# Kernel optimization log

Measured on AMD Instinct MI355X. Metric: run time of the kernel, lower is better.

## Reference

```python
import jax, jax.numpy as jnp
import numpy as np

D = 512      # model_dim
H = 8        # num_heads
HD = D // H  # head_dim = 64
S = 196      # tokens per channel (14x14 grid)
CHANNELS = np.array([2, 4, 6, 4], dtype=np.int32)  # multiplex channels per sample


def setup_inputs() -> dict:
    key = jax.random.key(0)
    ks = jax.random.split(key, 8)
    C = int(CHANNELS.sum())  # 16
    n = lambda k, shp, s=1.0: jax.random.normal(k, shp, dtype=jnp.float32) * s
    return {
        "x_query": n(ks[0], (C, S, D)),
        "x_keyval": n(ks[1], (C, S, D)),
        "pos": n(ks[2], (C, S, D)),
        "channels": CHANNELS,
        "Wq": n(ks[3], (D, D), 0.02), "bq": jnp.zeros((D,), jnp.float32),
        "Wk": n(ks[4], (D, D), 0.02), "bk": jnp.zeros((D,), jnp.float32),
        "Wv": n(ks[5], (D, D), 0.02), "bv": jnp.zeros((D,), jnp.float32),
        "Wo": n(ks[6], (D, D), 0.02), "bo": jnp.zeros((D,), jnp.float32),
    }


def reference(x_query, x_keyval, pos, channels, Wq, bq, Wk, bk, Wv, bv, Wo, bo):
    C, S_, D_ = x_query.shape
    ch = np.asarray(channels)
    # segment id per packed token; segment i has length channels[i]*S (== cu_seq_len blocks)
    seg = np.repeat(np.arange(ch.shape[0]), ch * S_)                # [T] static
    block_mask = seg[:, None] == seg[None, :]                        # [T,T] static bool

    xq = x_query.reshape(-1, D_)   # [T,D]
    xk = x_keyval.reshape(-1, D_)
    p = pos.reshape(-1, D_)

    # positional embedding fused into Q/K before projection (query_pos/key_pos)
    q = ((xq + p) @ Wq + bq).reshape(-1, H, HD)
    k = ((xk + p) @ Wk + bk).reshape(-1, H, HD)
    v = (xk @ Wv + bv).reshape(-1, H, HD)

    scale = 1.0 / np.sqrt(HD)
    scores = jnp.einsum('qhd,khd->hqk', q, k) * scale               # [H,T,T]
    scores = jnp.where(block_mask[None], scores, jnp.float32(-1e30))
    attn = jax.nn.softmax(scores, axis=-1)
    out = jnp.einsum('hqk,khd->qhd', attn, v).reshape(-1, D_)       # [T,D]
    out = out @ Wo + bo
    return out.reshape(C, S_, D_)
```

## Files before the change

kernel.cpp:

```cpp
#include <hip/hip_runtime.h>
#include <hip/hip_bf16.h>


typedef short short8 __attribute__((ext_vector_type(8)));
typedef float f32x4 __attribute__((ext_vector_type(4)));
typedef unsigned short ushort4v __attribute__((ext_vector_type(4)));

__device__ __forceinline__ unsigned short f2b(float f) {
    union { float f; unsigned int i; } x; x.f = f;
    unsigned int r = x.i + 0x7fffu + ((x.i >> 16) & 1u);
    return (unsigned short)(r >> 16);
}

#define NE 1605632
#define WE 262144
#define GS 72
#define LDA 520
#define TT 3136

__launch_bounds__(256)
__global__ void prep(const float* __restrict__ W0, const float* __restrict__ W1,
                     const float* __restrict__ W2, const float* __restrict__ W3,
                     unsigned short* __restrict__ WF) {
    const int tid = threadIdx.x;
    const float* W = blockIdx.z == 0 ? W0 : blockIdx.z == 1 ? W1 : blockIdx.z == 2 ? W2 : W3;
    unsigned short* T = WF + (size_t)blockIdx.z * WE;
    const int s = blockIdx.x * 4 + (tid >> 6);
    const int f = s >> 4, t = s & 15;
    const int lane = tid & 63, quad = lane >> 4, l16 = lane & 15;
    short8 o;
    #pragma unroll
    for (int j = 0; j < 8; ++j)
        o[j] = (short)f2b(W[(size_t)(t * 32 + quad * 8 + j) * 512 + f * 16 + l16]);
    *(short8*)(T + (size_t)s * 512 + lane * 8) = o;
}

__launch_bounds__(512)
__global__ void qkv_gemm(const float* __restrict__ xq, const float* __restrict__ xk,
                         const float* __restrict__ pos,
                         const unsigned short* __restrict__ WF,
                         const float* __restrict__ bq, const float* __restrict__ bk,
                         const float* __restrict__ bv,
                         unsigned short* __restrict__ qb, unsigned short* __restrict__ kb,
                         unsigned short* __restrict__ vb) {
    __shared__ __align__(16) unsigned short As[32 * LDA];

    const int z = blockIdx.z;
    const float* X = (z == 0) ? xq : xk;
    const bool addp = (z < 2);
    const unsigned short* WFw = WF + (size_t)z * WE;
    const float* bias = (z == 0) ? bq : (z == 1) ? bk : bv;
    unsigned short* C = (z == 0) ? qb : (z == 1) ? kb : vb;

    const int m0 = blockIdx.x * 32;
    const int tid = threadIdx.x;

    #pragma unroll
    for (int p = 0; p < 4; ++p) {
        const int row = p * 8 + (tid >> 6);
        const int col = (tid & 63) * 8;
        const float* src = X + (size_t)(m0 + row) * 512 + col;
        f32x4 a = *(const f32x4*)(src);
        f32x4 b = *(const f32x4*)(src + 4);
        if (addp) {
            const float* ps = pos + (size_t)(m0 + row) * 512 + col;
            f32x4 pa = *(const f32x4*)(ps), pb = *(const f32x4*)(ps + 4);
            #pragma unroll
            for (int j = 0; j < 4; ++j) { a[j] += pa[j]; b[j] += pb[j]; }
        }
        short8 o;
        #pragma unroll
        for (int j = 0; j < 4; ++j) {
            o[j] = (short)f2b(a[j]); o[4 + j] = (short)f2b(b[j]);
        }
        *(short8*)(As + row * LDA + col) = o;
    }
    __syncthreads();

    const int wave = tid >> 6, lane = tid & 63;
    const int quad = lane >> 4, l16 = lane & 15;
    const int n0 = wave * 64;
    const unsigned short* Ar0 = As + l16 * LDA + quad * 8;
    const unsigned short* Bb = WFw + (size_t)lane * 8 + (size_t)n0 * 512;

    f32x4 acc0[4] = {}, acc1[4] = {};
    short8 a0 = *(const short8*)(Ar0);
    short8 a1 = *(const short8*)(Ar0 + 16 * LDA);
    short8 b0 = *(const short8*)(Bb);
    short8 b1 = *(const short8*)(Bb + (size_t)16 * 512);
    short8 b2 = *(const short8*)(Bb + (size_t)32 * 512);
    short8 b3 = *(const short8*)(Bb + (size_t)48 * 512);
    #pragma unroll
    for (int t = 0; t < 16; ++t) {
        short8 na0, na1, nb0, nb1, nb2, nb3;
        if (t < 15) {
            na0 = *(const short8*)(Ar0 + (t + 1) * 32);
            na1 = *(const short8*)(Ar0 + 16 * LDA + (t + 1) * 32);
            nb0 = *(const short8*)(Bb + (size_t)(t + 1) * 512);
            nb1 = *(const short8*)(Bb + (size_t)(16 + t + 1) * 512);
            nb2 = *(const short8*)(Bb + (size_t)(32 + t + 1) * 512);
            nb3 = *(const short8*)(Bb + (size_t)(48 + t + 1) * 512);
        }
        acc0[0] = __builtin_amdgcn_mfma_f32_16x16x32_bf16(a0, b0, acc0[0], 0, 0, 0);
        acc1[0] = __builtin_amdgcn_mfma_f32_16x16x32_bf16(a1, b0, acc1[0], 0, 0, 0);
        acc0[1] = __builtin_amdgcn_mfma_f32_16x16x32_bf16(a0, b1, acc0[1], 0, 0, 0);
        acc1[1] = __builtin_amdgcn_mfma_f32_16x16x32_bf16(a1, b1, acc1[1], 0, 0, 0);
        acc0[2] = __builtin_amdgcn_mfma_f32_16x16x32_bf16(a0, b2, acc0[2], 0, 0, 0);
        acc1[2] = __builtin_amdgcn_mfma_f32_16x16x32_bf16(a1, b2, acc1[2], 0, 0, 0);
        acc0[3] = __builtin_amdgcn_mfma_f32_16x16x32_bf16(a0, b3, acc0[3], 0, 0, 0);
        acc1[3] = __builtin_amdgcn_mfma_f32_16x16x32_bf16(a1, b3, acc1[3], 0, 0, 0);
        a0 = na0; a1 = na1; b0 = nb0; b1 = nb1; b2 = nb2; b3 = nb3;
    }
    if (z == 2) {
        #pragma unroll
        for (int nt = 0; nt < 4; ++nt) {
            const int col = n0 + nt * 16 + l16;
            const float bv2 = bias[col];
            ushort4v w0, w1;
            #pragma unroll
            for (int r = 0; r < 4; ++r) {
                w0[r] = f2b(acc0[nt][r] + bv2);
                w1[r] = f2b(acc1[nt][r] + bv2);
            }
            *(ushort4v*)(C + (size_t)col * TT + m0 + quad * 4)      = w0;
            *(ushort4v*)(C + (size_t)col * TT + m0 + 16 + quad * 4) = w1;
        }
    } else {
        #pragma unroll
        for (int nt = 0; nt < 4; ++nt) {
            const int col = n0 + nt * 16 + l16;
            const float bv2 = bias[col];
            #pragma unroll
            for (int r = 0; r < 4; ++r) {
                const int row = m0 + quad * 4 + r;
                C[(size_t)row * 512 + col]        = f2b(acc0[nt][r] + bv2);
                C[(size_t)(row + 16) * 512 + col] = f2b(acc1[nt][r] + bv2);
            }
        }
    }
}

__launch_bounds__(256)
__global__ void out_gemm(const unsigned short* __restrict__ A,
                         const unsigned short* __restrict__ WFo,
                         const float* __restrict__ bo, float* __restrict__ out) {
    const int tid = threadIdx.x;
    const int wave = tid >> 6, lane = tid & 63;
    const int quad = lane >> 4, l16 = lane & 15;
    const int rg = wave & 1, cq = wave >> 1;
    const int m0 = blockIdx.x * 64 + rg * 32;
    const int n0 = blockIdx.y * 128 + cq * 64;
    const unsigned short* Ar0 = A + (size_t)(m0 + l16) * 512 + quad * 8;
    const unsigned short* Bb = WFo + (size_t)lane * 8 + (size_t)n0 * 512;

    f32x4 acc0[4] = {}, acc1[4] = {};
    short8 a0 = *(const short8*)(Ar0);
    short8 a1 = *(const short8*)(Ar0 + 16 * 512);
    short8 b0 = *(const short8*)(Bb);
    short8 b1 = *(const short8*)(Bb + (size_t)16 * 512);
    short8 b2 = *(const short8*)(Bb + (size_t)32 * 512);
    short8 b3 = *(const short8*)(Bb + (size_t)48 * 512);
    #pragma unroll
    for (int t = 0; t < 16; ++t) {
        short8 na0, na1, nb0, nb1, nb2, nb3;
        if (t < 15) {
            na0 = *(const short8*)(Ar0 + (t + 1) * 32);
            na1 = *(const short8*)(Ar0 + 16 * 512 + (t + 1) * 32);
            nb0 = *(const short8*)(Bb + (size_t)(t + 1) * 512);
            nb1 = *(const short8*)(Bb + (size_t)(16 + t + 1) * 512);
            nb2 = *(const short8*)(Bb + (size_t)(32 + t + 1) * 512);
            nb3 = *(const short8*)(Bb + (size_t)(48 + t + 1) * 512);
        }
        acc0[0] = __builtin_amdgcn_mfma_f32_16x16x32_bf16(a0, b0, acc0[0], 0, 0, 0);
        acc1[0] = __builtin_amdgcn_mfma_f32_16x16x32_bf16(a1, b0, acc1[0], 0, 0, 0);
        acc0[1] = __builtin_amdgcn_mfma_f32_16x16x32_bf16(a0, b1, acc0[1], 0, 0, 0);
        acc1[1] = __builtin_amdgcn_mfma_f32_16x16x32_bf16(a1, b1, acc1[1], 0, 0, 0);
        acc0[2] = __builtin_amdgcn_mfma_f32_16x16x32_bf16(a0, b2, acc0[2], 0, 0, 0);
        acc1[2] = __builtin_amdgcn_mfma_f32_16x16x32_bf16(a1, b2, acc1[2], 0, 0, 0);
        acc0[3] = __builtin_amdgcn_mfma_f32_16x16x32_bf16(a0, b3, acc0[3], 0, 0, 0);
        acc1[3] = __builtin_amdgcn_mfma_f32_16x16x32_bf16(a1, b3, acc1[3], 0, 0, 0);
        a0 = na0; a1 = na1; b0 = nb0; b1 = nb1; b2 = nb2; b3 = nb3;
    }
    #pragma unroll
    for (int nt = 0; nt < 4; ++nt) {
        const int col = n0 + nt * 16 + l16;
        const float bv = bo[col];
        #pragma unroll
        for (int r = 0; r < 4; ++r) {
            const int row = m0 + quad * 4 + r;
            out[(size_t)row * 512 + col]        = acc0[nt][r] + bv;
            out[(size_t)(row + 16) * 512 + col] = acc1[nt][r] + bv;
        }
    }
}

__launch_bounds__(512)
__global__ void attn_seg(const unsigned short* __restrict__ q,
                         const unsigned short* __restrict__ k,
                         const unsigned short* __restrict__ vt,
                         unsigned short* __restrict__ o) {
    __shared__ __align__(16) unsigned char Lds[55296];

    const int id = blockIdx.x;
    int h, off, L, qt;
    if (id < 152)      { h = id & 7; qt = id >> 3; off = 1176; L = 1176; }
    else if (id < 360) { int m = id - 152; h = m & 7; int s = m >> 3;
                         if (s < 13) { off = 392;  L = 784; qt = s; }
                         else        { off = 2352; L = 784; qt = s - 13; } }
    else               { int m = id - 360; h = m & 7; qt = m >> 3; off = 0; L = 392; }

    const int tid = threadIdx.x;
    const int wave = tid >> 6, lane = tid & 63;
    const int grp = wave >> 2, w4 = wave & 3;
    const int quad = lane >> 4, l16 = lane & 15;
    const int hb = h * 64;
    const int lastr = off + L - 1;

    unsigned short* Ks = (unsigned short*)(Lds + grp * 18432);
    unsigned short* Vt = (unsigned short*)(Lds + grp * 18432 + 9216);
    unsigned char*  Pme = Lds + 36864 + wave * 2304;

    int qrow = off + qt * 64 + w4 * 16 + l16;
    if (qrow > lastr) qrow = lastr;
    const short8 qf0 = *(const short8*)(q + (size_t)qrow * 512 + hb + quad * 8);
    const short8 qf1 = *(const short8*)(q + (size_t)qrow * 512 + hb + 32 + quad * 8);

    const int skey = lane, sd = w4 * 16;
    const unsigned short* vrow = vt + (size_t)(hb + lane) * TT + off;
    const int ntiles = (L + 63) >> 6;
    const int nt0 = (ntiles + 1) >> 1;

    float lsum = 0.f;
    f32x4 oacc[4] = {};

    short8 kr0, kr1, vs0, vs1;
    {
        const int tb = (grp ? nt0 : 0) * 64;
        int kk = tb + skey;
        int krow = off + (kk < L ? kk : L - 1);
        kr0 = *(const short8*)(k + (size_t)krow * 512 + hb + sd);
        kr1 = *(const short8*)(k + (size_t)krow * 512 + hb + sd + 8);
        int c0 = tb + w4 * 16;     if (c0 + 8 > L) c0 = L - 8;
        int c1 = tb + w4 * 16 + 8; if (c1 + 8 > L) c1 = L - 8;
        vs0 = *(const short8*)(vrow + c0);
        vs1 = *(const short8*)(vrow + c1);
    }
    unsigned char* pwr = Pme + l16 * 144 + quad * 8;
    const unsigned char* prd = Pme + l16 * 144 + quad * 16;

    for (int i = 0; i < nt0; ++i) {
        const int tg = (grp ? nt0 : 0) + i;
        __syncthreads();
        *(short8*)(Ks + skey * GS + sd)     = kr0;
        *(short8*)(Ks + skey * GS + sd + 8) = kr1;
        *(short8*)(Vt + lane * GS + w4 * 16)     = vs0;
        *(short8*)(Vt + lane * GS + w4 * 16 + 8) = vs1;
        __syncthreads();
        if (i + 1 < nt0) {
            const int tb = (tg + 1) * 64;
            int kk = tb + skey;
            int krow = off + (kk < L ? kk : L - 1);
            kr0 = *(const short8*)(k + (size_t)krow * 512 + hb + sd);
            kr1 = *(const short8*)(k + (size_t)krow * 512 + hb + sd + 8);
            int c0 = tb + w4 * 16;     if (c0 + 8 > L) c0 = L - 8;
            int c1 = tb + w4 * 16 + 8; if (c1 + 8 > L) c1 = L - 8;
            vs0 = *(const short8*)(vrow + c0);
            vs1 = *(const short8*)(vrow + c1);
        }
        f32x4 sT[4];
        __builtin_amdgcn_s_setprio(1);
        #pragma unroll
        for (int g = 0; g < 4; ++g) {
            short8 kb0 = *(const short8*)(Ks + (g * 16 + l16) * GS + quad * 8);
            short8 kb1 = *(const short8*)(Ks + (g * 16 + l16) * GS + 32 + quad * 8);
            f32x4 z = {0.f, 0.f, 0.f, 0.f};
            z     = __builtin_amdgcn_mfma_f32_16x16x32_bf16(kb0, qf0, z, 0, 0, 0);
            sT[g] = __builtin_amdgcn_mfma_f32_16x16x32_bf16(kb1, qf1, z, 0, 0, 0);
        }
        __builtin_amdgcn_s_setprio(0);
        const int kbase = tg * 64 + quad * 4;
        #pragma unroll
        for (int g = 0; g < 4; ++g) {
            float p[4];
            #pragma unroll
            for (int r = 0; r < 4; ++r) {
                const bool valid = (kbase + g * 16 + r) < L;
                p[r] = valid ? __expf(fminf(sT[g][r] * 0.125f, 30.f)) : 0.f;
                lsum += p[r];
            }
            #pragma unroll
            for (int i2 = 0; i2 < 2; ++i2) {
                __hip_bfloat162 t = __float22bfloat162_rn(make_float2(p[2 * i2], p[2 * i2 + 1]));
                *(unsigned int*)(pwr + g * 32 + i2 * 4) = *(unsigned int*)&t;
            }
        }
        short8 pa0 = *(const short8*)(prd);
        short8 pa1 = *(const short8*)(prd + 64);
        __builtin_amdgcn_s_setprio(1);
        #pragma unroll
        for (int nt = 0; nt < 4; ++nt) {
            short8 vf0 = *(const short8*)(Vt + (nt * 16 + l16) * GS + quad * 8);
            short8 vf1 = *(const short8*)(Vt + (nt * 16 + l16) * GS + 32 + quad * 8);
            oacc[nt] = __builtin_amdgcn_mfma_f32_16x16x32_bf16(pa0, vf0, oacc[nt], 0, 0, 0);
            oacc[nt] = __builtin_amdgcn_mfma_f32_16x16x32_bf16(pa1, vf1, oacc[nt], 0, 0, 0);
        }
        __builtin_amdgcn_s_setprio(0);
    }
    lsum += __shfl_xor(lsum, 16);
    lsum += __shfl_xor(lsum, 32);

    __syncthreads();
    float* Mrg = (float*)(Lds + w4 * 5120 + lane * 80);
    float* Ls  = (float*)(Lds + 20480);
    if (grp == 1) {
        #pragma unroll
        for (int nt = 0; nt < 4; ++nt) *(f32x4*)(Mrg + nt * 4) = oacc[nt];
        Ls[w4 * 64 + lane] = lsum;
    }
    __syncthreads();
    if (grp == 0) {
        lsum += Ls[w4 * 64 + lane];
        #pragma unroll
        for (int nt = 0; nt < 4; ++nt) {
            f32x4 po = *(const f32x4*)(Mrg + nt * 4);
            oacc[nt] += po;
        }
        #pragma unroll
        for (int r = 0; r < 4; ++r) {
            const float srow = __shfl(lsum, (lane & 48) + quad * 4 + r);
            const float linv = 1.0f / srow;
            const int qi = qt * 64 + w4 * 16 + quad * 4 + r;
            if (qi < L) {
                #pragma unroll
                for (int nt = 0; nt < 4; ++nt)
                    o[(size_t)(off + qi) * 512 + hb + nt * 16 + l16] = f2b(oacc[nt][r] * linv);
            }
        }
    }
}

extern "C" void kernel_launch(void* const* d_in, const int* in_sizes, int n_in,
                              void* d_out, int out_size, void* d_ws, size_t ws_size,
                              hipStream_t stream) {
    const float* xq  = (const float*)d_in[0];
    const float* xk  = (const float*)d_in[1];
    const float* pos = (const float*)d_in[2];
    const float* Wq = (const float*)d_in[4];
    const float* bq = (const float*)d_in[5];
    const float* Wk = (const float*)d_in[6];
    const float* bk = (const float*)d_in[7];
    const float* Wv = (const float*)d_in[8];
    const float* bv = (const float*)d_in[9];
    const float* Wo = (const float*)d_in[10];
    const float* bo = (const float*)d_in[11];
    float* out = (float*)d_out;

    unsigned short* ws = (unsigned short*)d_ws;
    unsigned short* qb = ws;
    unsigned short* kb = ws + NE;
    unsigned short* vb = ws + (size_t)2 * NE;
    unsigned short* WF = ws + (size_t)3 * NE;

    prep<<<dim3(128, 1, 4), 256, 0, stream>>>(Wq, Wk, Wv, Wo, WF);
    qkv_gemm<<<dim3(98, 1, 3), 512, 0, stream>>>(xq, xk, pos, WF, bq, bk, bv,
                                                 qb, kb, vb);
    attn_seg<<<dim3(416), 512, 0, stream>>>(qb, kb, vb, qb);
    out_gemm<<<dim3(49, 4), 256, 0, stream>>>(qb, WF + (size_t)3 * WE, bo, out);
}
```

Before: 135.1 us.

## Fuse output projection into attention via per-window atomic counters

Removes the separate out_gemm launch. Each attention block bumps an atomic counter for its 64-row query window, and the last of the 8 head blocks to finish runs the output projection for that window, reading the attention output from global memory. The counters are zeroed by an extra z-slice of the prep kernel. This saves a kernel launch and lets the projection overlap with attention still running elsewhere. In exchange, only 52 blocks do the projection, each covering 64 rows by 512 columns, so the tail work is serialized on few CUs and depends on fences for correctness.

```diff
diff --git a/kernel.cpp b/kernel.cpp
--- a/kernel.cpp
+++ b/kernel.cpp
@@ -21,8 +21,12 @@
 __launch_bounds__(256)
 __global__ void prep(const float* __restrict__ W0, const float* __restrict__ W1,
                      const float* __restrict__ W2, const float* __restrict__ W3,
-                     unsigned short* __restrict__ WF) {
+                     unsigned short* __restrict__ WF, int* __restrict__ cnt) {
     const int tid = threadIdx.x;
+    if (blockIdx.z == 4) {
+        if (blockIdx.x == 0 && tid < 52) cnt[tid] = 0;
+        return;
+    }
     const float* W = blockIdx.z == 0 ? W0 : blockIdx.z == 1 ? W1 : blockIdx.z == 2 ? W2 : W3;
     unsigned short* T = WF + (size_t)blockIdx.z * WE;
     const int s = blockIdx.x * 4 + (tid >> 6);
@@ -140,74 +144,24 @@
     }
 }
 
-__launch_bounds__(256)
-__global__ void out_gemm(const unsigned short* __restrict__ A,
-                         const unsigned short* __restrict__ WFo,
-                         const float* __restrict__ bo, float* __restrict__ out) {
-    const int tid = threadIdx.x;
-    const int wave = tid >> 6, lane = tid & 63;
-    const int quad = lane >> 4, l16 = lane & 15;
-    const int rg = wave & 1, cq = wave >> 1;
-    const int m0 = blockIdx.x * 64 + rg * 32;
-    const int n0 = blockIdx.y * 128 + cq * 64;
-    const unsigned short* Ar0 = A + (size_t)(m0 + l16) * 512 + quad * 8;
-    const unsigned short* Bb = WFo + (size_t)lane * 8 + (size_t)n0 * 512;
-
-    f32x4 acc0[4] = {}, acc1[4] = {};
-    short8 a0 = *(const short8*)(Ar0);
-    short8 a1 = *(const short8*)(Ar0 + 16 * 512);
-    short8 b0 = *(const short8*)(Bb);
-    short8 b1 = *(const short8*)(Bb + (size_t)16 * 512);
-    short8 b2 = *(const short8*)(Bb + (size_t)32 * 512);
-    short8 b3 = *(const short8*)(Bb + (size_t)48 * 512);
-    #pragma unroll
-    for (int t = 0; t < 16; ++t) {
-        short8 na0, na1, nb0, nb1, nb2, nb3;
-        if (t < 15) {
-            na0 = *(const short8*)(Ar0 + (t + 1) * 32);
-            na1 = *(const short8*)(Ar0 + 16 * 512 + (t + 1) * 32);
-            nb0 = *(const short8*)(Bb + (size_t)(t + 1) * 512);
-            nb1 = *(const short8*)(Bb + (size_t)(16 + t + 1) * 512);
-            nb2 = *(const short8*)(Bb + (size_t)(32 + t + 1) * 512);
-            nb3 = *(const short8*)(Bb + (size_t)(48 + t + 1) * 512);
-        }
-        acc0[0] = __builtin_amdgcn_mfma_f32_16x16x32_bf16(a0, b0, acc0[0], 0, 0, 0);
-        acc1[0] = __builtin_amdgcn_mfma_f32_16x16x32_bf16(a1, b0, acc1[0], 0, 0, 0);
-        acc0[1] = __builtin_amdgcn_mfma_f32_16x16x32_bf16(a0, b1, acc0[1], 0, 0, 0);
-        acc1[1] = __builtin_amdgcn_mfma_f32_16x16x32_bf16(a1, b1, acc1[1], 0, 0, 0);
-        acc0[2] = __builtin_amdgcn_mfma_f32_16x16x32_bf16(a0, b2, acc0[2], 0, 0, 0);
-        acc1[2] = __builtin_amdgcn_mfma_f32_16x16x32_bf16(a1, b2, acc1[2], 0, 0, 0);
-        acc0[3] = __builtin_amdgcn_mfma_f32_16x16x32_bf16(a0, b3, acc0[3], 0, 0, 0);
-        acc1[3] = __builtin_amdgcn_mfma_f32_16x16x32_bf16(a1, b3, acc1[3], 0, 0, 0);
-        a0 = na0; a1 = na1; b0 = nb0; b1 = nb1; b2 = nb2; b3 = nb3;
-    }
-    #pragma unroll
-    for (int nt = 0; nt < 4; ++nt) {
-        const int col = n0 + nt * 16 + l16;
-        const float bv = bo[col];
-        #pragma unroll
-        for (int r = 0; r < 4; ++r) {
-            const int row = m0 + quad * 4 + r;
-            out[(size_t)row * 512 + col]        = acc0[nt][r] + bv;
-            out[(size_t)(row + 16) * 512 + col] = acc1[nt][r] + bv;
-        }
-    }
-}
-
 __launch_bounds__(512)
 __global__ void attn_seg(const unsigned short* __restrict__ q,
                          const unsigned short* __restrict__ k,
                          const unsigned short* __restrict__ vt,
-                         unsigned short* __restrict__ o) {
+                         unsigned short* __restrict__ o,
+                         const unsigned short* __restrict__ WFo,
+                         const float* __restrict__ bo,
+                         float* __restrict__ out,
+                         int* __restrict__ cnt) {
     __shared__ __align__(16) unsigned char Lds[55296];
 
     const int id = blockIdx.x;
-    int h, off, L, qt;
-    if (id < 152)      { h = id & 7; qt = id >> 3; off = 1176; L = 1176; }
+    int h, off, L, qt, win;
+    if (id < 152)      { h = id & 7; qt = id >> 3; off = 1176; L = 1176; win = 20 + qt; }
     else if (id < 360) { int m = id - 152; h = m & 7; int s = m >> 3;
-                         if (s < 13) { off = 392;  L = 784; qt = s; }
-                         else        { off = 2352; L = 784; qt = s - 13; } }
-    else               { int m = id - 360; h = m & 7; qt = m >> 3; off = 0; L = 392; }
+                         if (s < 13) { off = 392;  L = 784; qt = s;      win = 7 + s; }
+                         else        { off = 2352; L = 784; qt = s - 13; win = 39 + (s - 13); } }
+    else               { int m = id - 360; h = m & 7; qt = m >> 3; off = 0; L = 392; win = qt; }
 
     const int tid = threadIdx.x;
     const int wave = tid >> 6, lane = tid & 63;
@@ -337,6 +291,57 @@
             }
         }
     }
+
+    __syncthreads();
+    if (tid == 0) {
+        __threadfence();
+        int old = atomicAdd(cnt + win, 1);
+        *(int*)Lds = (old == 7);
+    }
+    __syncthreads();
+    if (*(int*)Lds == 0) return;
+    __threadfence();
+
+    const int win_start = off + qt * 64;
+    const int len = min(64, L - qt * 64);
+    const int n0 = wave * 64;
+    int arr = w4 * 0;
+    (void)arr;
+    const unsigned short* Bb = WFo + (size_t)lane * 8 + (size_t)n0 * 512;
+    f32x4 acc[4][4] = {};
+    int rowv[4];
+    #pragma unroll
+    for (int rg = 0; rg < 4; ++rg) {
+        int rr = rg * 16 + l16;
+        rowv[rg] = win_start + (rr < len ? rr : 0);
+    }
+    for (int t = 0; t < 16; ++t) {
+        short8 a[4];
+        #pragma unroll
+        for (int rg = 0; rg < 4; ++rg)
+            a[rg] = *(const short8*)(o + (size_t)rowv[rg] * 512 + t * 32 + quad * 8);
+        #pragma unroll
+        for (int f = 0; f < 4; ++f) {
+            short8 b = *(const short8*)(Bb + (size_t)(f * 16 + t) * 512);
+            #pragma unroll
+            for (int rg = 0; rg < 4; ++rg)
+                acc[rg][f] = __builtin_amdgcn_mfma_f32_16x16x32_bf16(a[rg], b, acc[rg][f], 0, 0, 0);
+        }
+    }
+    #pragma unroll
+    for (int f = 0; f < 4; ++f) {
+        const int col = n0 + f * 16 + l16;
+        const float bv = bo[col];
+        #pragma unroll
+        for (int rg = 0; rg < 4; ++rg) {
+            #pragma unroll
+            for (int r = 0; r < 4; ++r) {
+                const int rr = rg * 16 + quad * 4 + r;
+                if (rr < len)
+                    out[(size_t)(win_start + rr) * 512 + col] = acc[rg][f][r] + bv;
+            }
+        }
+    }
 }
 
 extern "C" void kernel_launch(void* const* d_in, const int* in_sizes, int n_in,
@@ -360,10 +365,11 @@
     unsigned short* kb = ws + NE;
     unsigned short* vb = ws + (size_t)2 * NE;
     unsigned short* WF = ws + (size_t)3 * NE;
-
-    prep<<<dim3(128, 1, 4), 256, 0, stream>>>(Wq, Wk, Wv, Wo, WF);
+    int* cnt = (int*)(ws + (size_t)3 * NE + (size_t)4 * WE);
+
+    prep<<<dim3(128, 1, 5), 256, 0, stream>>>(Wq, Wk, Wv, Wo, WF, cnt);
     qkv_gemm<<<dim3(98, 1, 3), 512, 0, stream>>>(xq, xk, pos, WF, bq, bk, bv,
                                                  qb, kb, vb);
-    attn_seg<<<dim3(416), 512, 0, stream>>>(qb, kb, vb, qb);
-    out_gemm<<<dim3(49, 4), 256, 0, stream>>>(qb, WF + (size_t)3 * WE, bo, out);
-}
+    attn_seg<<<dim3(416), 512, 0, stream>>>(qb, kb, vb, qb,
+                                            WF + (size_t)3 * WE, bo, out, cnt);
+}
```

After: 246.8 us. 82.7% more time.
